# Kernel tuning notes

Hardware: AMD Instinct MI355X
Metric: run time of the kernel (lower is better)

The kernel has to match this reference:

```python
import jax, jax.numpy as jnp
import numpy as np

B, T = 256, 32
V, E, H = 10000, 512, 512


def setup_inputs() -> dict:
    key = jax.random.key(0)
    ks = jax.random.split(key, 9)
    s = 0.05
    return {
        "caps": jax.random.randint(ks[0], (B, T), 0, V),
        "latent": jax.random.normal(ks[1], (B, H), dtype=jnp.float32),
        "embed": jax.random.normal(ks[2], (V, E), dtype=jnp.float32) * s,
        "W_ih": jax.random.normal(ks[3], (4 * H, E), dtype=jnp.float32) * s,
        "W_hh": jax.random.normal(ks[4], (4 * H, H), dtype=jnp.float32) * s,
        "b_ih": jax.random.normal(ks[5], (4 * H,), dtype=jnp.float32) * s,
        "b_hh": jax.random.normal(ks[6], (4 * H,), dtype=jnp.float32) * s,
        "W_lin": jax.random.normal(ks[7], (V, H), dtype=jnp.float32) * s,
        "b_lin": jax.random.normal(ks[8], (V,), dtype=jnp.float32) * s,
    }


def reference(caps, latent, embed, W_ih, W_hh, b_ih, b_hh, W_lin, b_lin):
    # Teacher-forced decoder (train_bool=True): step i consumes caps[:, i-1],
    # writes logits into outputs[i]; outputs[0] stays zero.
    bias = b_ih + b_hh  # [4H]

    def step(carry, tok):
        h, c = carry  # [B,H] each
        x = embed[tok]  # [B,E]
        gates = x @ W_ih.T + h @ W_hh.T + bias  # [B,4H], PyTorch gate order i,f,g,o
        i_g, f_g, g_g, o_g = jnp.split(gates, 4, axis=-1)
        c = jax.nn.sigmoid(f_g) * c + jax.nn.sigmoid(i_g) * jnp.tanh(g_g)
        h = jax.nn.sigmoid(o_g) * jnp.tanh(c)
        logits = h @ W_lin.T + b_lin  # [B,V]
        return (h, c), logits

    h0 = latent
    c0 = jnp.zeros_like(latent)
    tokens = caps[:, :-1].T  # [T-1, B]: inputs for steps 1..T-1
    _, outs = jax.lax.scan(step, (h0, c0), tokens)  # [T-1, B, V]
    zero_row = jnp.zeros((1,) + outs.shape[1:], dtype=outs.dtype)
    return jnp.concatenate([zero_row, outs], axis=0)  # [T, B, V]
```

## Files before the change

kernel.cpp:

```cpp
#include <hip/hip_runtime.h>
#include <hip/hip_bf16.h>
#include <stdint.h>

#define B_    256
#define T_    32
#define V_    10000
#define E_    512
#define H_    512
#define NSTEP 31
#define M_    7936
#define NG_   2048
#define VPAD_ 10240

typedef __attribute__((ext_vector_type(8))) short  short8;
typedef __attribute__((ext_vector_type(4))) float  f32x4;

static __device__ __forceinline__ unsigned short f2bf(float f) {
  __hip_bfloat16 h = __float2bfloat16(f);
  return *reinterpret_cast<unsigned short*>(&h);
}
static __device__ __forceinline__ ushort4 f4_to_bf4(float4 a) {
  ushort4 r; r.x = f2bf(a.x); r.y = f2bf(a.y); r.z = f2bf(a.z); r.w = f2bf(a.w); return r;
}
static __device__ __forceinline__ float fsig(float x) {
  return 1.f / (1.f + __expf(-x));
}
static __device__ __forceinline__ float ftanh_(float x) {
  x = fminf(fmaxf(x, -30.f), 30.f);
  float e = __expf(-2.f * x);
  return (1.f - e) / (1.f + e);
}

#define GLOAD_LDS16(gp, lp)                                                                   \
  __builtin_amdgcn_global_load_lds((const __attribute__((address_space(1))) unsigned int*)(gp), \
                                   (__attribute__((address_space(3))) unsigned int*)(lp), 16, 0, 0)

static __device__ __forceinline__ void store8_cc(void* p, uint2 v) {
  asm volatile("global_store_dwordx2 %0, %1, off sc0 sc1" :: "v"(p), "v"(v) : "memory");
}

__global__ __launch_bounds__(256) void k_prep(
    const float* __restrict__ Wih, const float* __restrict__ Whh,
    const float* __restrict__ Wlin, const float* __restrict__ bih,
    const float* __restrict__ bhh,
    unsigned short* __restrict__ Wihb, unsigned short* __restrict__ Whhb,
    unsigned short* __restrict__ Wlb, float* __restrict__ bias) {
  const int stride = gridDim.x * 256;
  const int i0 = blockIdx.x * 256 + threadIdx.x;
  for (int q = i0; q < (NG_ * E_) / 4; q += stride) {
    ((ushort4*)Wihb)[q] = f4_to_bf4(((const float4*)Wih)[q]);
    ((ushort4*)Whhb)[q] = f4_to_bf4(((const float4*)Whh)[q]);
  }
  for (int q = i0; q < (VPAD_ * H_) / 4; q += stride) {
    int row = q >> 7;
    ushort4 r;
    if (row < V_) r = f4_to_bf4(((const float4*)Wlin)[q]);
    else { r.x = 0; r.y = 0; r.z = 0; r.w = 0; }
    ((ushort4*)Wlb)[q] = r;
  }
  for (int q = i0; q < NG_; q += stride) bias[q] = bih[q] + bhh[q];
}

__global__ __launch_bounds__(256) void k_gather(
    const int* __restrict__ caps, const float* __restrict__ embed,
    const float* __restrict__ latent,
    unsigned short* __restrict__ Xbf, unsigned short* __restrict__ HsAll,
    float* __restrict__ out0, int* __restrict__ cnt) {
  const int stride = gridDim.x * 256;
  const int i0 = blockIdx.x * 256 + threadIdx.x;
  for (int q = i0; q < (M_ * E_) / 4; q += stride) {
    int m = q >> 7;
    int e4 = q & 127;
    int t = m >> 8, b = m & 255;
    int tok = caps[b * T_ + t];
    float4 a = ((const float4*)(embed + (size_t)tok * E_))[e4];
    ((ushort4*)Xbf)[q] = f4_to_bf4(a);
  }
  for (int q = i0; q < (B_ * H_) / 4; q += stride)
    ((ushort4*)HsAll)[q] = f4_to_bf4(((const float4*)latent)[q]);
  float4 z = make_float4(0.f, 0.f, 0.f, 0.f);
  for (int q = i0; q < (B_ * V_) / 4; q += stride)
    ((float4*)out0)[q] = z;
  if (blockIdx.x == 0 && threadIdx.x < 32 * 8)
    cnt[threadIdx.x] = 0;
}

template<bool NT>
__global__ __launch_bounds__(512, 2) void gemm256(
    const unsigned short* __restrict__ A, const unsigned short* __restrict__ Bt,
    const float* __restrict__ bias, float* __restrict__ Out, int ldo, int Nvalid) {
  __shared__ unsigned short As[2 * 256 * 64];
  __shared__ unsigned short Bs[2 * 256 * 64];
  const int tid = threadIdx.x;
  const int w = tid >> 6, l = tid & 63;
  const int wr = w >> 2, wc = w & 3;

  int flat = blockIdx.y * gridDim.x + blockIdx.x;
  int nwg = gridDim.x * gridDim.y;
  int tile = flat;
  if ((nwg & 7) == 0) { int cpx = nwg >> 3; tile = (flat & 7) * cpx + (flat >> 3); }
  const int bm = tile / gridDim.x, bn = tile % gridDim.x;

  const int srow = (w << 3) + (l >> 3);
  const int schunk = (l & 7) ^ ((l >> 3) & 7);
  const unsigned short* Ab = A + (size_t)(bm * 256 + srow) * 512 + (schunk << 3);
  const unsigned short* Bb = Bt + (size_t)(bn * 256 + srow) * 512 + (schunk << 3);
  unsigned short* Al = As + (w << 9);
  unsigned short* Bl = Bs + (w << 9);

  f32x4 acc[8][4] = {};
  const int lr = l & 15;

#pragma unroll
  for (int i = 0; i < 4; ++i) {
    GLOAD_LDS16(Ab + (size_t)(i << 6) * 512, Al + (i << 12));
    GLOAD_LDS16(Bb + (size_t)(i << 6) * 512, Bl + (i << 12));
  }
  asm volatile("s_waitcnt vmcnt(0)" ::: "memory");
  __syncthreads();

  for (int t = 0; t < 8; ++t) {
    const int cur = (t & 1) << 14;
    if (t < 7) {
      const int nb = ((t & 1) ^ 1) << 14;
      const int k0 = (t + 1) << 6;
#pragma unroll
      for (int i = 0; i < 4; ++i) {
        GLOAD_LDS16(Ab + (size_t)(i << 6) * 512 + k0, Al + nb + (i << 12));
        GLOAD_LDS16(Bb + (size_t)(i << 6) * 512 + k0, Bl + nb + (i << 12));
      }
    }
    const unsigned short* ab = As + cur;
    const unsigned short* bb = Bs + cur;
#pragma unroll
    for (int kc = 0; kc < 2; ++kc) {
      const int cI = (kc << 2) + (l >> 4);
      const int rchunk = (cI ^ (lr & 7)) << 3;
      short8 af[8], bf8[4];
#pragma unroll
      for (int m = 0; m < 8; ++m)
        af[m] = *(const short8*)(ab + ((wr << 7) + (m << 4) + lr) * 64 + rchunk);
#pragma unroll
      for (int n = 0; n < 4; ++n)
        bf8[n] = *(const short8*)(bb + ((wc << 6) + (n << 4) + lr) * 64 + rchunk);
#pragma unroll
      for (int m = 0; m < 8; ++m)
#pragma unroll
        for (int n = 0; n < 4; ++n)
          acc[m][n] = __builtin_amdgcn_mfma_f32_16x16x32_bf16(af[m], bf8[n], acc[m][n], 0, 0, 0);
    }
    asm volatile("s_waitcnt vmcnt(0)" ::: "memory");
    __syncthreads();
  }

  const int orow0 = bm * 256 + (wr << 7) + ((l >> 4) << 2);
  const int ocol0 = bn * 256 + (wc << 6) + lr;
#pragma unroll
  for (int n = 0; n < 4; ++n) {
    int col = ocol0 + (n << 4);
    if (col < Nvalid) {
      float bv = bias[col];
#pragma unroll
      for (int m = 0; m < 8; ++m) {
        int row = orow0 + (m << 4);
#pragma unroll
        for (int r = 0; r < 4; ++r) {
          float v = acc[m][n][r] + bv;
          float* p = &Out[(size_t)(row + r) * ldo + col];
          if (NT) __builtin_nontemporal_store(v, p);
          else    *p = v;
        }
      }
    }
  }
}

__global__ __launch_bounds__(512, 2) void k_mix(
    const float* __restrict__ Xg,
    const unsigned short* __restrict__ Whhb,
    const unsigned short* __restrict__ Wlb,
    const float* __restrict__ blin,
    unsigned short* __restrict__ HsAll,
    int* __restrict__ cnt,
    float* __restrict__ out) {
  __shared__ uint4 smem_raw[131072 / 16];
  const int tid = threadIdx.x;
  const int w = tid >> 6, l = tid & 63;
  const int lr = l & 15;

  if (blockIdx.x < 64) {
    unsigned short* hsh = (unsigned short*)smem_raw;
    float* gsh = (float*)((char*)smem_raw + 32768);
    const int gb = blockIdx.x & 7;
    const int ct = blockIdx.x >> 3;
    const int b0 = gb << 5;
    const int n0 = ct << 6;
    const int g  = w >> 1;
    const int cs = (w & 1) << 5;
    const int lk = (l >> 4) << 3;

    short8 bf0[16], bf1[16];
    {
      const unsigned short* wb0 = Whhb + (size_t)(g * 512 + n0 + cs + lr) * 512 + lk;
      const unsigned short* wb1 = wb0 + (size_t)16 * 512;
#pragma unroll 16
      for (int ks = 0; ks < 16; ++ks) {
        bf0[ks] = *(const short8*)(wb0 + (ks << 5));
        bf1[ks] = *(const short8*)(wb1 + (ks << 5));
      }
    }
    float c_reg[4] = {0.f, 0.f, 0.f, 0.f};
    const int br  = tid >> 4;
    const int nc0 = (tid & 15) << 2;
    const size_t xg_base = ((size_t)(b0 + br) << 11) + n0 + nc0;

    for (int t = 0; t < NSTEP; ++t) {
      const f32x4* xp = (const f32x4*)(Xg + (size_t)t * B_ * NG_ + xg_base);
      f32x4 xiv = xp[0], xfv = xp[128], xgv = xp[256], xov = xp[384];

      if (t > 0) {
        int ok;
        do {
          int val = 1;
          if (tid == 0)
            val = (__hip_atomic_load(&cnt[t * 8 + gb], __ATOMIC_RELAXED,
                                     __HIP_MEMORY_SCOPE_AGENT) == 8);
          ok = __syncthreads_and(val);
          if (!ok) __builtin_amdgcn_s_sleep(2);
        } while (!ok);
      }

#pragma unroll
      for (int j = 0; j < 4; ++j) {
        int row = (j << 3) + w;
        const unsigned short* gsrc = HsAll + (size_t)t * B_ * H_ +
                                     (size_t)(b0 + row) * 512 + ((l ^ (row & 7)) << 3);
        GLOAD_LDS16(gsrc, hsh + row * 512);
      }
      __syncthreads();

      f32x4 acc[2][2] = {};
#pragma unroll
      for (int ks = 0; ks < 16; ++ks) {
        int kc = (ks << 2) + (l >> 4);
        short8 a0 = *(const short8*)(hsh + lr * 512 + ((kc ^ (lr & 7)) << 3));
        short8 a1 = *(const short8*)(hsh + (16 + lr) * 512 + ((kc ^ (lr & 7)) << 3));
        acc[0][0] = __builtin_amdgcn_mfma_f32_16x16x32_bf16(a0, bf0[ks], acc[0][0], 0, 0, 0);
        acc[0][1] = __builtin_amdgcn_mfma_f32_16x16x32_bf16(a0, bf1[ks], acc[0][1], 0, 0, 0);
        acc[1][0] = __builtin_amdgcn_mfma_f32_16x16x32_bf16(a1, bf0[ks], acc[1][0], 0, 0, 0);
        acc[1][1] = __builtin_amdgcn_mfma_f32_16x16x32_bf16(a1, bf1[ks], acc[1][1], 0, 0, 0);
      }

      const int gr0 = (l >> 4) << 2;
#pragma unroll
      for (int m = 0; m < 2; ++m)
#pragma unroll
        for (int n = 0; n < 2; ++n)
#pragma unroll
          for (int r = 0; r < 4; ++r)
            gsh[g * 2048 + (m * 16 + gr0 + r) * 64 + cs + n * 16 + lr] = acc[m][n][r];
      __syncthreads();

      f32x4 giv = *(const f32x4*)&gsh[0 * 2048 + br * 64 + nc0];
      f32x4 gfv = *(const f32x4*)&gsh[1 * 2048 + br * 64 + nc0];
      f32x4 ggv = *(const f32x4*)&gsh[2 * 2048 + br * 64 + nc0];
      f32x4 gov = *(const f32x4*)&gsh[3 * 2048 + br * 64 + nc0];
      ushort4 hv; unsigned short* hvp = &hv.x;
#pragma unroll
      for (int j = 0; j < 4; ++j) {
        float is = fsig(giv[j] + xiv[j]);
        float fs = fsig(gfv[j] + xfv[j]);
        float os = fsig(gov[j] + xov[j]);
        float gt = ftanh_(ggv[j] + xgv[j]);
        float cn = fs * c_reg[j] + is * gt;
        c_reg[j] = cn;
        hvp[j] = f2bf(os * ftanh_(cn));
      }
      unsigned short* h_out = HsAll + (size_t)(t + 1) * B_ * H_;
      store8_cc(h_out + ((size_t)(b0 + br) << 9) + n0 + nc0,
                *reinterpret_cast<uint2*>(&hv));

      asm volatile("s_waitcnt vmcnt(0)" ::: "memory");
      __syncthreads();
      if (tid == 0)
        __hip_atomic_fetch_add(&cnt[(t + 1) * 8 + gb], 1, __ATOMIC_RELAXED,
                               __HIP_MEMORY_SCOPE_AGENT);
    }
  } else {
    unsigned short* As = (unsigned short*)smem_raw;
    unsigned short* Bs = (unsigned short*)((char*)smem_raw + 65536);
    const int idx = blockIdx.x - 64;
    const int t  = idx / 40 + 1;
    const int bn = idx % 40;

    {
      int ok;
      do {
        int val = 1;
        if (tid < 8)
          val = (__hip_atomic_load(&cnt[t * 8 + tid], __ATOMIC_RELAXED,
                                   __HIP_MEMORY_SCOPE_AGENT) == 8);
        ok = __syncthreads_and(val);
        if (!ok) __builtin_amdgcn_s_sleep(16);
      } while (!ok);
    }

    const unsigned short* slotT = HsAll + (size_t)t * B_ * H_;
    const int wr = w >> 2, wc = w & 3;
    const int srow = (w << 3) + (l >> 3);
    const int schunk = (l & 7) ^ ((l >> 3) & 7);
    const unsigned short* Ab = slotT + (size_t)srow * 512 + (schunk << 3);
    const unsigned short* Bb = Wlb + (size_t)(bn * 256 + srow) * 512 + (schunk << 3);
    unsigned short* Al = As + (w << 9);
    unsigned short* Bl = Bs + (w << 9);

    f32x4 acc[8][4] = {};
#pragma unroll
    for (int i = 0; i < 4; ++i) {
      GLOAD_LDS16(Ab + (size_t)(i << 6) * 512, Al + (i << 12));
      GLOAD_LDS16(Bb + (size_t)(i << 6) * 512, Bl + (i << 12));
    }
    asm volatile("s_waitcnt vmcnt(0)" ::: "memory");
    __syncthreads();

    for (int kt = 0; kt < 8; ++kt) {
      const int cur = (kt & 1) << 14;
      if (kt < 7) {
        const int nb = ((kt & 1) ^ 1) << 14;
        const int k0 = (kt + 1) << 6;
#pragma unroll
        for (int i = 0; i < 4; ++i) {
          GLOAD_LDS16(Ab + (size_t)(i << 6) * 512 + k0, Al + nb + (i << 12));
          GLOAD_LDS16(Bb + (size_t)(i << 6) * 512 + k0, Bl + nb + (i << 12));
        }
      }
      const unsigned short* ab = As + cur;
      const unsigned short* bb = Bs + cur;
#pragma unroll
      for (int kc = 0; kc < 2; ++kc) {
        const int cI = (kc << 2) + (l >> 4);
        const int rchunk = (cI ^ (lr & 7)) << 3;
        short8 af[8], bf8[4];
#pragma unroll
        for (int m = 0; m < 8; ++m)
          af[m] = *(const short8*)(ab + ((wr << 7) + (m << 4) + lr) * 64 + rchunk);
#pragma unroll
        for (int n = 0; n < 4; ++n)
          bf8[n] = *(const short8*)(bb + ((wc << 6) + (n << 4) + lr) * 64 + rchunk);
#pragma unroll
        for (int m = 0; m < 8; ++m)
#pragma unroll
          for (int n = 0; n < 4; ++n)
            acc[m][n] = __builtin_amdgcn_mfma_f32_16x16x32_bf16(af[m], bf8[n], acc[m][n], 0, 0, 0);
      }
      asm volatile("s_waitcnt vmcnt(0)" ::: "memory");
      __syncthreads();
    }

    const int orow0 = t * 256 + (wr << 7) + ((l >> 4) << 2);
    const int ocol0 = bn * 256 + (wc << 6) + lr;
#pragma unroll
    for (int n = 0; n < 4; ++n) {
      int col = ocol0 + (n << 4);
      if (col < V_) {
        float bv = blin[col];
#pragma unroll
        for (int m = 0; m < 8; ++m) {
          int row = orow0 + (m << 4);
#pragma unroll
          for (int r = 0; r < 4; ++r)
            __builtin_nontemporal_store(acc[m][n][r] + bv,
                &out[(size_t)(row + r) * V_ + col]);
        }
      }
    }
  }
}

extern "C" void kernel_launch(void* const* d_in, const int* in_sizes, int n_in,
                              void* d_out, int out_size, void* d_ws, size_t ws_size,
                              hipStream_t stream) {
  const int*   caps   = (const int*)d_in[0];
  const float* latent = (const float*)d_in[1];
  const float* embed  = (const float*)d_in[2];
  const float* Wih    = (const float*)d_in[3];
  const float* Whh    = (const float*)d_in[4];
  const float* bih    = (const float*)d_in[5];
  const float* bhh    = (const float*)d_in[6];
  const float* Wlin   = (const float*)d_in[7];
  const float* blin   = (const float*)d_in[8];
  float* out = (float*)d_out;

  char* ws = (char*)d_ws;
  size_t off = 0;
  auto alloc = [&](size_t bytes) {
    void* p = ws + off;
    off = (off + bytes + 255) & ~(size_t)255;
    return p;
  };
  unsigned short* Xbf   = (unsigned short*)alloc((size_t)M_ * E_ * 2);
  unsigned short* Wihb  = (unsigned short*)alloc((size_t)NG_ * E_ * 2);
  unsigned short* Whhb  = (unsigned short*)alloc((size_t)NG_ * H_ * 2);
  unsigned short* Wlb   = (unsigned short*)alloc((size_t)VPAD_ * H_ * 2);
  float*          bias  = (float*)alloc((size_t)NG_ * 4);
  float*          Xg    = (float*)alloc((size_t)M_ * NG_ * 4);
  unsigned short* HsAll = (unsigned short*)alloc((size_t)(NSTEP + 1) * B_ * H_ * 2);
  int*            cnt   = (int*)alloc((size_t)32 * 8 * 4);
  (void)ws_size; (void)in_sizes; (void)n_in; (void)out_size;

  hipLaunchKernelGGL(k_prep, dim3(2048), dim3(256), 0, stream,
                     Wih, Whh, Wlin, bih, bhh, Wihb, Whhb, Wlb, bias);
  hipLaunchKernelGGL(k_gather, dim3(2048), dim3(256), 0, stream,
                     caps, embed, latent, Xbf, HsAll, out, cnt);
  hipLaunchKernelGGL((gemm256<false>), dim3(NG_ / 256, M_ / 256), dim3(512), 0, stream,
                     Xbf, Wihb, bias, Xg, NG_, NG_);
  hipLaunchKernelGGL(k_mix, dim3(64 + NSTEP * 40), dim3(512), 0, stream,
                     Xg, Whhb, Wlb, blin, HsAll, cnt, out);
}
```

Measured before the change: 224.7 us.

## Fuse input-projection GEMM into persistent LSTM kernel with per-step readiness counters

Merges the prep and gather kernels into one init kernel, and moves the X·W_ih input-projection GEMM into the main mixed kernel as a third class of workgroups. These workgroups signal per-timestep completion through a new counter array that the recurrent chain blocks poll before reading each step's gate inputs. The aim is to overlap the large input GEMM with the sequential recurrence and logits work, and to remove two kernel launches. The cost is extra polling, coherent stores to Xg, and a reliance on the GEMM blocks being scheduled early enough that the chain blocks do not stall or deadlock.

```diff
diff --git a/kernel.cpp b/kernel.cpp
--- a/kernel.cpp
+++ b/kernel.cpp
@@ -12,6 +12,12 @@
 #define NG_   2048
 #define VPAD_ 10240
 
+#define NCHAIN   64
+#define NXG      248
+#define XG_BASE  NCHAIN
+#define LG_BASE  (NCHAIN + NXG)
+#define NLOGIT   (NSTEP * 40)
+
 typedef __attribute__((ext_vector_type(8))) short  short8;
 typedef __attribute__((ext_vector_type(4))) float  f32x4;
 
@@ -38,13 +44,20 @@
 static __device__ __forceinline__ void store8_cc(void* p, uint2 v) {
   asm volatile("global_store_dwordx2 %0, %1, off sc0 sc1" :: "v"(p), "v"(v) : "memory");
 }
-
-__global__ __launch_bounds__(256) void k_prep(
+static __device__ __forceinline__ void storef_cc(float* p, float v) {
+  asm volatile("global_store_dword %0, %1, off sc0 sc1" :: "v"(p), "v"(v) : "memory");
+}
+
+__global__ __launch_bounds__(256) void k_init(
+    const int* __restrict__ caps, const float* __restrict__ embed,
+    const float* __restrict__ latent,
     const float* __restrict__ Wih, const float* __restrict__ Whh,
     const float* __restrict__ Wlin, const float* __restrict__ bih,
     const float* __restrict__ bhh,
     unsigned short* __restrict__ Wihb, unsigned short* __restrict__ Whhb,
-    unsigned short* __restrict__ Wlb, float* __restrict__ bias) {
+    unsigned short* __restrict__ Wlb, float* __restrict__ bias,
+    unsigned short* __restrict__ Xbf, unsigned short* __restrict__ HsAll,
+    float* __restrict__ out0, int* __restrict__ cntbuf) {
   const int stride = gridDim.x * 256;
   const int i0 = blockIdx.x * 256 + threadIdx.x;
   for (int q = i0; q < (NG_ * E_) / 4; q += stride) {
@@ -59,15 +72,6 @@
     ((ushort4*)Wlb)[q] = r;
   }
   for (int q = i0; q < NG_; q += stride) bias[q] = bih[q] + bhh[q];
-}
-
-__global__ __launch_bounds__(256) void k_gather(
-    const int* __restrict__ caps, const float* __restrict__ embed,
-    const float* __restrict__ latent,
-    unsigned short* __restrict__ Xbf, unsigned short* __restrict__ HsAll,
-    float* __restrict__ out0, int* __restrict__ cnt) {
-  const int stride = gridDim.x * 256;
-  const int i0 = blockIdx.x * 256 + threadIdx.x;
   for (int q = i0; q < (M_ * E_) / 4; q += stride) {
     int m = q >> 7;
     int e4 = q & 127;
@@ -81,114 +85,28 @@
   float4 z = make_float4(0.f, 0.f, 0.f, 0.f);
   for (int q = i0; q < (B_ * V_) / 4; q += stride)
     ((float4*)out0)[q] = z;
-  if (blockIdx.x == 0 && threadIdx.x < 32 * 8)
-    cnt[threadIdx.x] = 0;
-}
-
-template<bool NT>
-__global__ __launch_bounds__(512, 2) void gemm256(
-    const unsigned short* __restrict__ A, const unsigned short* __restrict__ Bt,
-    const float* __restrict__ bias, float* __restrict__ Out, int ldo, int Nvalid) {
-  __shared__ unsigned short As[2 * 256 * 64];
-  __shared__ unsigned short Bs[2 * 256 * 64];
-  const int tid = threadIdx.x;
-  const int w = tid >> 6, l = tid & 63;
-  const int wr = w >> 2, wc = w & 3;
-
-  int flat = blockIdx.y * gridDim.x + blockIdx.x;
-  int nwg = gridDim.x * gridDim.y;
-  int tile = flat;
-  if ((nwg & 7) == 0) { int cpx = nwg >> 3; tile = (flat & 7) * cpx + (flat >> 3); }
-  const int bm = tile / gridDim.x, bn = tile % gridDim.x;
-
-  const int srow = (w << 3) + (l >> 3);
-  const int schunk = (l & 7) ^ ((l >> 3) & 7);
-  const unsigned short* Ab = A + (size_t)(bm * 256 + srow) * 512 + (schunk << 3);
-  const unsigned short* Bb = Bt + (size_t)(bn * 256 + srow) * 512 + (schunk << 3);
-  unsigned short* Al = As + (w << 9);
-  unsigned short* Bl = Bs + (w << 9);
-
-  f32x4 acc[8][4] = {};
-  const int lr = l & 15;
-
-#pragma unroll
-  for (int i = 0; i < 4; ++i) {
-    GLOAD_LDS16(Ab + (size_t)(i << 6) * 512, Al + (i << 12));
-    GLOAD_LDS16(Bb + (size_t)(i << 6) * 512, Bl + (i << 12));
-  }
-  asm volatile("s_waitcnt vmcnt(0)" ::: "memory");
-  __syncthreads();
-
-  for (int t = 0; t < 8; ++t) {
-    const int cur = (t & 1) << 14;
-    if (t < 7) {
-      const int nb = ((t & 1) ^ 1) << 14;
-      const int k0 = (t + 1) << 6;
-#pragma unroll
-      for (int i = 0; i < 4; ++i) {
-        GLOAD_LDS16(Ab + (size_t)(i << 6) * 512 + k0, Al + nb + (i << 12));
-        GLOAD_LDS16(Bb + (size_t)(i << 6) * 512 + k0, Bl + nb + (i << 12));
-      }
-    }
-    const unsigned short* ab = As + cur;
-    const unsigned short* bb = Bs + cur;
-#pragma unroll
-    for (int kc = 0; kc < 2; ++kc) {
-      const int cI = (kc << 2) + (l >> 4);
-      const int rchunk = (cI ^ (lr & 7)) << 3;
-      short8 af[8], bf8[4];
-#pragma unroll
-      for (int m = 0; m < 8; ++m)
-        af[m] = *(const short8*)(ab + ((wr << 7) + (m << 4) + lr) * 64 + rchunk);
-#pragma unroll
-      for (int n = 0; n < 4; ++n)
-        bf8[n] = *(const short8*)(bb + ((wc << 6) + (n << 4) + lr) * 64 + rchunk);
-#pragma unroll
-      for (int m = 0; m < 8; ++m)
-#pragma unroll
-        for (int n = 0; n < 4; ++n)
-          acc[m][n] = __builtin_amdgcn_mfma_f32_16x16x32_bf16(af[m], bf8[n], acc[m][n], 0, 0, 0);
-    }
-    asm volatile("s_waitcnt vmcnt(0)" ::: "memory");
-    __syncthreads();
-  }
-
-  const int orow0 = bm * 256 + (wr << 7) + ((l >> 4) << 2);
-  const int ocol0 = bn * 256 + (wc << 6) + lr;
-#pragma unroll
-  for (int n = 0; n < 4; ++n) {
-    int col = ocol0 + (n << 4);
-    if (col < Nvalid) {
-      float bv = bias[col];
-#pragma unroll
-      for (int m = 0; m < 8; ++m) {
-        int row = orow0 + (m << 4);
-#pragma unroll
-        for (int r = 0; r < 4; ++r) {
-          float v = acc[m][n][r] + bv;
-          float* p = &Out[(size_t)(row + r) * ldo + col];
-          if (NT) __builtin_nontemporal_store(v, p);
-          else    *p = v;
-        }
-      }
-    }
-  }
+  if (i0 < 256 + 32)
+    cntbuf[i0] = 0;
 }
 
 __global__ __launch_bounds__(512, 2) void k_mix(
-    const float* __restrict__ Xg,
+    const unsigned short* __restrict__ Xbf,
+    const unsigned short* __restrict__ Wihb,
+    const float* __restrict__ bias,
+    float* __restrict__ Xg,
     const unsigned short* __restrict__ Whhb,
     const unsigned short* __restrict__ Wlb,
     const float* __restrict__ blin,
     unsigned short* __restrict__ HsAll,
     int* __restrict__ cnt,
+    int* __restrict__ xcnt,
     float* __restrict__ out) {
   __shared__ uint4 smem_raw[131072 / 16];
   const int tid = threadIdx.x;
   const int w = tid >> 6, l = tid & 63;
   const int lr = l & 15;
 
-  if (blockIdx.x < 64) {
+  if (blockIdx.x < NCHAIN) {
     unsigned short* hsh = (unsigned short*)smem_raw;
     float* gsh = (float*)((char*)smem_raw + 32768);
     const int gb = blockIdx.x & 7;
@@ -215,14 +133,14 @@
     const size_t xg_base = ((size_t)(b0 + br) << 11) + n0 + nc0;
 
     for (int t = 0; t < NSTEP; ++t) {
-      const f32x4* xp = (const f32x4*)(Xg + (size_t)t * B_ * NG_ + xg_base);
-      f32x4 xiv = xp[0], xfv = xp[128], xgv = xp[256], xov = xp[384];
-
-      if (t > 0) {
+      {
         int ok;
         do {
           int val = 1;
           if (tid == 0)
+            val = (__hip_atomic_load(&xcnt[t], __ATOMIC_RELAXED,
+                                     __HIP_MEMORY_SCOPE_AGENT) == 8);
+          else if (tid == 64 && t > 0)
             val = (__hip_atomic_load(&cnt[t * 8 + gb], __ATOMIC_RELAXED,
                                      __HIP_MEMORY_SCOPE_AGENT) == 8);
           ok = __syncthreads_and(val);
@@ -237,6 +155,8 @@
                                      (size_t)(b0 + row) * 512 + ((l ^ (row & 7)) << 3);
         GLOAD_LDS16(gsrc, hsh + row * 512);
       }
+      const f32x4* xp = (const f32x4*)(Xg + (size_t)t * B_ * NG_ + xg_base);
+      f32x4 xiv = xp[0], xfv = xp[128], xgv = xp[256], xov = xp[384];
       __syncthreads();
 
       f32x4 acc[2][2] = {};
@@ -286,10 +206,86 @@
         __hip_atomic_fetch_add(&cnt[(t + 1) * 8 + gb], 1, __ATOMIC_RELAXED,
                                __HIP_MEMORY_SCOPE_AGENT);
     }
+  } else if (blockIdx.x < LG_BASE) {
+    unsigned short* As = (unsigned short*)smem_raw;
+    unsigned short* Bs = (unsigned short*)((char*)smem_raw + 65536);
+    const int idx = blockIdx.x - XG_BASE;
+    const int bm = idx >> 3;
+    const int bn = idx & 7;
+    const int wr = w >> 2, wc = w & 3;
+    const int srow = (w << 3) + (l >> 3);
+    const int schunk = (l & 7) ^ ((l >> 3) & 7);
+    const unsigned short* Ab = Xbf + (size_t)(bm * 256 + srow) * 512 + (schunk << 3);
+    const unsigned short* Bb = Wihb + (size_t)(bn * 256 + srow) * 512 + (schunk << 3);
+    unsigned short* Al = As + (w << 9);
+    unsigned short* Bl = Bs + (w << 9);
+
+    f32x4 acc[8][4] = {};
+#pragma unroll
+    for (int i = 0; i < 4; ++i) {
+      GLOAD_LDS16(Ab + (size_t)(i << 6) * 512, Al + (i << 12));
+      GLOAD_LDS16(Bb + (size_t)(i << 6) * 512, Bl + (i << 12));
+    }
+    asm volatile("s_waitcnt vmcnt(0)" ::: "memory");
+    __syncthreads();
+
+    for (int kt = 0; kt < 8; ++kt) {
+      const int cur = (kt & 1) << 14;
+      if (kt < 7) {
+        const int nb = ((kt & 1) ^ 1) << 14;
+        const int k0 = (kt + 1) << 6;
+#pragma unroll
+        for (int i = 0; i < 4; ++i) {
+          GLOAD_LDS16(Ab + (size_t)(i << 6) * 512 + k0, Al + nb + (i << 12));
+          GLOAD_LDS16(Bb + (size_t)(i << 6) * 512 + k0, Bl + nb + (i << 12));
+        }
+      }
+      const unsigned short* ab = As + cur;
+      const unsigned short* bb = Bs + cur;
+#pragma unroll
+      for (int kc = 0; kc < 2; ++kc) {
+        const int cI = (kc << 2) + (l >> 4);
+        const int rchunk = (cI ^ (lr & 7)) << 3;
+        short8 af[8], bf8[4];
+#pragma unroll
+        for (int m = 0; m < 8; ++m)
+          af[m] = *(const short8*)(ab + ((wr << 7) + (m << 4) + lr) * 64 + rchunk);
+#pragma unroll
+        for (int n = 0; n < 4; ++n)
+          bf8[n] = *(const short8*)(bb + ((wc << 6) + (n << 4) + lr) * 64 + rchunk);
+#pragma unroll
+        for (int m = 0; m < 8; ++m)
+#pragma unroll
+          for (int n = 0; n < 4; ++n)
+            acc[m][n] = __builtin_amdgcn_mfma_f32_16x16x32_bf16(af[m], bf8[n], acc[m][n], 0, 0, 0);
+      }
+      asm volatile("s_waitcnt vmcnt(0)" ::: "memory");
+      __syncthreads();
+    }
+
+    const int orow0 = bm * 256 + (wr << 7) + ((l >> 4) << 2);
+    const int ocol0 = bn * 256 + (wc << 6) + lr;
+#pragma unroll
+    for (int n = 0; n < 4; ++n) {
+      int col = ocol0 + (n << 4);
+      float bv = bias[col];
+#pragma unroll
+      for (int m = 0; m < 8; ++m) {
+        int row = orow0 + (m << 4);
+#pragma unroll
+        for (int r = 0; r < 4; ++r)
+          storef_cc(&Xg[(size_t)(row + r) * NG_ + col], acc[m][n][r] + bv);
+      }
+    }
+    asm volatile("s_waitcnt vmcnt(0)" ::: "memory");
+    __syncthreads();
+    if (tid == 0)
+      __hip_atomic_fetch_add(&xcnt[bm], 1, __ATOMIC_RELAXED,
+                             __HIP_MEMORY_SCOPE_AGENT);
   } else {
     unsigned short* As = (unsigned short*)smem_raw;
     unsigned short* Bs = (unsigned short*)((char*)smem_raw + 65536);
-    const int idx = blockIdx.x - 64;
+    const int idx = blockIdx.x - LG_BASE;
     const int t  = idx / 40 + 1;
     const int bn = idx % 40;
 
@@ -301,7 +297,7 @@
           val = (__hip_atomic_load(&cnt[t * 8 + tid], __ATOMIC_RELAXED,
                                    __HIP_MEMORY_SCOPE_AGENT) == 8);
         ok = __syncthreads_and(val);
-        if (!ok) __builtin_amdgcn_s_sleep(16);
+        if (!ok) __builtin_amdgcn_s_sleep(32);
       } while (!ok);
     }
 
@@ -405,15 +401,14 @@
   float*          bias  = (float*)alloc((size_t)NG_ * 4);
   float*          Xg    = (float*)alloc((size_t)M_ * NG_ * 4);
   unsigned short* HsAll = (unsigned short*)alloc((size_t)(NSTEP + 1) * B_ * H_ * 2);
-  int*            cnt   = (int*)alloc((size_t)32 * 8 * 4);
+  int*            cntb  = (int*)alloc((size_t)(256 + 32) * 4);
+  int* cnt  = cntb;
+  int* xcnt = cntb + 256;
   (void)ws_size; (void)in_sizes; (void)n_in; (void)out_size;
 
-  hipLaunchKernelGGL(k_prep, dim3(2048), dim3(256), 0, stream,
-                     Wih, Whh, Wlin, bih, bhh, Wihb, Whhb, Wlb, bias);
-  hipLaunchKernelGGL(k_gather, dim3(2048), dim3(256), 0, stream,
-                     caps, embed, latent, Xbf, HsAll, out, cnt);
-  hipLaunchKernelGGL((gemm256<false>), dim3(NG_ / 256, M_ / 256), dim3(512), 0, stream,
-                     Xbf, Wihb, bias, Xg, NG_, NG_);
-  hipLaunchKernelGGL(k_mix, dim3(64 + NSTEP * 40), dim3(512), 0, stream,
-                     Xg, Whhb, Wlb, blin, HsAll, cnt, out);
-}
+  hipLaunchKernelGGL(k_init, dim3(2048), dim3(256), 0, stream,
+                     caps, embed, latent, Wih, Whh, Wlin, bih, bhh,
+                     Wihb, Whhb, Wlb, bias, Xbf, HsAll, out, cntb);
+  hipLaunchKernelGGL(k_mix, dim3(NCHAIN + NXG + NLOGIT), dim3(512), 0, stream,
+                     Xbf, Wihb, bias, Xg, Whhb, Wlb, blin, HsAll, cnt, xcnt, out);
+}
```

Result: no change. 226.5 us (+0.8%).
